# Optimization experiments

Hardware: AMD Instinct MI355X
Metric: run time of the kernel (lower is better)

The kernel has to match this reference:

```python
import jax, jax.numpy as jnp
import numpy as np

N = 8192      # num nodes
E = 131072    # num edges (avg degree 16)
B = 2         # batch
F_NODE = 128
F_EDGE = 64
H = 256       # hidden_dim
L = 3         # num_layers


def setup_inputs() -> dict:
    key = jax.random.key(0)
    ks = jax.random.split(key, 16)
    # unique edges, sorted row-major to match the original i-then-j loop order
    rng = np.random.default_rng(0)
    lin = np.sort(rng.choice(N * N, size=E, replace=False))
    src = jnp.asarray(lin // N, dtype=jnp.int32)
    dst = jnp.asarray(lin % N, dtype=jnp.int32)
    adjacency = jnp.zeros((N, N), jnp.float32).at[src, dst].set(1.0)

    s = 0.05
    return {
        "node_features": jax.random.normal(ks[0], (B, N, F_NODE), jnp.float32),
        "edge_features": jax.random.normal(ks[1], (B, E, F_EDGE), jnp.float32),
        "adjacency": adjacency,
        "src_idx": src,
        "dst_idx": dst,
        "W_ne": jax.random.normal(ks[2], (F_NODE, H), jnp.float32) * s,
        "b_ne": jnp.zeros((H,), jnp.float32),
        "W_ee": jax.random.normal(ks[3], (F_EDGE, H), jnp.float32) * s,
        "b_ee": jnp.zeros((H,), jnp.float32),
        "W_conv": jax.random.normal(ks[4], (L, H, H), jnp.float32) * s,
        "b_conv": jnp.zeros((L, H), jnp.float32),
        "W_cls": jax.random.normal(ks[5], (H, 5), jnp.float32) * s,
        "b_cls": jnp.zeros((5,), jnp.float32),
        "W_ep": jax.random.normal(ks[6], (2 * H, 1), jnp.float32) * s,
        "b_ep": jnp.zeros((1,), jnp.float32),
        "W_gp": jax.random.normal(ks[7], (H, 1), jnp.float32) * s,
        "b_gp": jnp.zeros((1,), jnp.float32),
    }


def reference(node_features, edge_features, adjacency, src_idx, dst_idx,
              W_ne, b_ne, W_ee, b_ee, W_conv, b_conv,
              W_cls, b_cls, W_ep, b_ep, W_gp, b_gp):
    # embeddings (eval mode: dropout is identity)
    h = jax.nn.relu(node_features @ W_ne + b_ne)          # [B,N,H]
    e = jax.nn.relu(edge_features @ W_ee + b_ee)          # [B,E,H] (computed, unused downstream as in original)
    # message-passing layers: messages = A @ h, then linear+relu+residual
    for l in range(L):
        m = jnp.einsum('ij,bjh->bih', adjacency, h)       # dense adjacency matmul
        o = jax.nn.relu(m @ W_conv[l] + b_conv[l])
        h = o + h                                          # residual (in==out dim)
    node_health = h @ W_cls + b_cls                        # [B,N,5]
    # fused edge prediction over all nonzero adjacency entries (row-major order)
    h_src = h[:, src_idx, :]                               # [B,E,H]
    h_dst = h[:, dst_idx, :]                               # [B,E,H]
    edge_repr = jnp.concatenate([h_src, h_dst], axis=-1)   # [B,E,2H]
    edge_propagation = jax.nn.sigmoid(edge_repr @ W_ep + b_ep)  # [B,E,1]
    global_repr = jnp.mean(h, axis=1)                      # [B,H]
    system_health = jax.nn.sigmoid(global_repr @ W_gp + b_gp)   # [B,1]
    return (node_health, edge_propagation, system_health, h)
```

## Files before the change

kernel.cpp:

```cpp
#include <hip/hip_runtime.h>
#include <hip/hip_bf16.h>

typedef __bf16 bf16_t;
typedef __bf16 bf16x8 __attribute__((ext_vector_type(8)));
typedef float f32x4 __attribute__((ext_vector_type(4)));

#define N_NODES 8192
#define N_EDGES 131072
#define HDIM    256


__device__ inline int rowblk_swz(int x) {
  int xcd = x & 7, q = x >> 3;
  return (xcd >> 2) * 128 + (xcd & 3) * 32 + q;
}

__device__ inline float wred(float v) {
#pragma unroll
  for (int m = 32; m; m >>= 1) v += __shfl_xor(v, m);
  return v;
}

__global__ __launch_bounds__(256) void gemm1_prep_k(const float* __restrict__ nf,
                                                    const float* __restrict__ Wne,
                                                    const float* __restrict__ bne,
                                                    const float* __restrict__ Wconv,
                                                    const int* __restrict__ src,
                                                    int* __restrict__ rp,
                                                    bf16_t* __restrict__ WconvT,
                                                    bf16_t* __restrict__ hs0) {
  __shared__ char smem[64 * 65 * 4];
  int x = blockIdx.x, tid = threadIdx.x;
  if (x >= 1024) {
    if (x < 1057) {
      int i = (x - 1024) * 256 + tid;
      if (i < N_NODES) {
        int lo = 0, hi = N_EDGES;
        while (lo < hi) { int mid = (lo + hi) >> 1; if (src[mid] < i) lo = mid + 1; else hi = mid; }
        rp[i] = lo;
      } else if (i == N_NODES) {
        rp[i] = N_EDGES;
      }
    } else {
      float (*tl)[65] = (float(*)[65])smem;
      int t = x - 1057;
      int l = t >> 4, tile = t & 15;
      int tr = (tile >> 2) * 64, tc = (tile & 3) * 64;
      int j = tid & 63, i0 = tid >> 6;
#pragma unroll
      for (int s = 0; s < 16; ++s) {
        int i = 4 * s + i0;
        tl[i][j] = Wconv[l * 65536 + (tr + i) * 256 + tc + j];
      }
      __syncthreads();
#pragma unroll
      for (int s = 0; s < 16; ++s) {
        int i = 4 * s + i0;
        WconvT[l * 65536 + (tc + i) * 256 + tr + j] = (bf16_t)tl[j][i];
      }
    }
    return;
  }
  bf16_t* Wlds = (bf16_t*)smem;
  int xb = x & 255, yb = x >> 8;
  int cg0 = yb * 64;
  for (int k = tid >> 6; k < 128; k += 4) {
    int lc = tid & 63;
    float w = Wne[k * 256 + cg0 + lc];
    Wlds[lc * 128 + (((k >> 3) ^ (lc & 15)) << 3) + (k & 7)] = (bf16_t)w;
  }
  int lane = tid & 63, wv = tid >> 6;
  int r0 = (rowblk_swz(xb) * 4 + wv) * 16;
  int l15 = lane & 15, l4 = lane >> 4;
  bf16x8 a[4];
  const float* Ap = nf + (size_t)(r0 + l15) * 128 + 8 * l4;
#pragma unroll
  for (int kk = 0; kk < 4; ++kk) {
    f32x4 a0 = *(const f32x4*)(Ap + 32 * kk);
    f32x4 a1 = *(const f32x4*)(Ap + 32 * kk + 4);
#pragma unroll
    for (int j = 0; j < 4; ++j) { a[kk][j] = (bf16_t)a0[j]; a[kk][4 + j] = (bf16_t)a1[j]; }
  }
  __syncthreads();
#pragma unroll
  for (int ct = 0; ct < 4; ++ct) {
    int lc0 = ct * 16;
    f32x4 acc = {0.f, 0.f, 0.f, 0.f};
#pragma unroll
    for (int kk = 0; kk < 4; ++kk) {
      bf16x8 b = *(const bf16x8*)&Wlds[(lc0 + l15) * 128 + (((4 * kk + l4) ^ l15) << 3)];
      acc = __builtin_amdgcn_mfma_f32_16x16x32_bf16(a[kk], b, acc, 0, 0, 0);
    }
    int col = cg0 + lc0 + l15;
    float bv = bne[col];
#pragma unroll
    for (int i = 0; i < 4; ++i) {
      int row = r0 + 4 * l4 + i;
      size_t idx = (size_t)row * HDIM + col;
      hs0[idx] = (bf16_t)fmaxf(acc[i] + bv, 0.f);
    }
  }
}

__global__ __launch_bounds__(512) void gconv_k(const bf16_t* __restrict__ hs_in,
                                               const int* __restrict__ rp,
                                               const int* __restrict__ dst,
                                               const bf16_t* __restrict__ BT,
                                               const float* __restrict__ bias,
                                               bf16_t* __restrict__ hs_out) {
  __shared__ bf16_t A_lds[32 * 256];
  int tid = threadIdx.x;
  int x = blockIdx.x;
  int xcd = x & 7, q = x >> 3;
  int b = xcd >> 2;
  int blk = (xcd & 3) * 64 + q;
  int i0 = blk * 32;
  int gang = tid >> 5, l32 = tid & 31;
  const bf16_t* hb = hs_in + (size_t)b * (N_NODES * HDIM) + l32 * 8;
#pragma unroll
  for (int r2 = 0; r2 < 2; ++r2) {
    int lrow = gang * 2 + r2;
    int i = i0 + lrow;
    int e0 = rp[i], e1 = rp[i + 1];
    float acc[8] = {0.f, 0.f, 0.f, 0.f, 0.f, 0.f, 0.f, 0.f};
    int e = e0;
    for (; e + 8 <= e1; e += 8) {
      bf16x8 v[8];
#pragma unroll
      for (int u = 0; u < 8; ++u) v[u] = *(const bf16x8*)(hb + (size_t)dst[e + u] * HDIM);
#pragma unroll
      for (int u = 0; u < 8; ++u)
#pragma unroll
        for (int jj = 0; jj < 8; ++jj) acc[jj] += (float)v[u][jj];
    }
    for (; e < e1; ++e) {
      bf16x8 v = *(const bf16x8*)(hb + (size_t)dst[e] * HDIM);
#pragma unroll
      for (int jj = 0; jj < 8; ++jj) acc[jj] += (float)v[jj];
    }
    bf16x8 o;
#pragma unroll
    for (int jj = 0; jj < 8; ++jj) o[jj] = (bf16_t)acc[jj];
    *(bf16x8*)&A_lds[lrow * 256 + ((l32 ^ (lrow & 7)) * 8)] = o;
  }
  __syncthreads();
  int lane = tid & 63, wv = tid >> 6;
  int wr = wv >> 2, wc = wv & 3;
  int l15 = lane & 15, l4 = lane >> 4;
  bf16x8 a[8];
#pragma unroll
  for (int kk = 0; kk < 8; ++kk)
    a[kk] = *(const bf16x8*)&A_lds[(wr * 16 + l15) * 256 + (((kk * 4 + l4) ^ (l15 & 7)) * 8)];
  int row_base = b * N_NODES + i0 + wr * 16;
#pragma unroll
  for (int ct = 0; ct < 4; ++ct) {
    int c0 = wc * 64 + ct * 16;
    const bf16_t* Bp = BT + (size_t)(c0 + l15) * HDIM + 8 * l4;
    f32x4 acc = {0.f, 0.f, 0.f, 0.f};
#pragma unroll
    for (int kk = 0; kk < 8; ++kk)
      acc = __builtin_amdgcn_mfma_f32_16x16x32_bf16(a[kk], *(const bf16x8*)(Bp + 32 * kk), acc, 0, 0, 0);
    int col = c0 + l15;
    float bv = bias[col];
#pragma unroll
    for (int ii = 0; ii < 4; ++ii) {
      int row = row_base + 4 * l4 + ii;
      size_t idx = (size_t)row * HDIM + col;
      float v = fmaxf(acc[ii] + bv, 0.f) + (float)hs_in[idx];
      hs_out[idx] = (bf16_t)v;
    }
  }
}

__global__ __launch_bounds__(512) void gconv_heads_k(const bf16_t* __restrict__ hs_in,
                                                     const int* __restrict__ rp,
                                                     const int* __restrict__ dst,
                                                     const bf16_t* __restrict__ BT,
                                                     const float* __restrict__ bias,
                                                     float* __restrict__ out_h,
                                                     const float* __restrict__ Wcls,
                                                     const float* __restrict__ bcls,
                                                     const float* __restrict__ Wep,
                                                     const float* __restrict__ Wgp,
                                                     float* __restrict__ ds,
                                                     float* __restrict__ dd,
                                                     float* __restrict__ pg,
                                                     float* __restrict__ out_nh) {
  __shared__ bf16_t A_lds[32 * 256];
  __shared__ float red[2][4][16][8];
  __shared__ float pgrow[32];
  int tid = threadIdx.x;
  int x = blockIdx.x;
  int xcd = x & 7, q = x >> 3;
  int b = xcd >> 2;
  int blk = (xcd & 3) * 64 + q;
  int i0 = blk * 32;
  int gang = tid >> 5, l32 = tid & 31;
  const bf16_t* hb = hs_in + (size_t)b * (N_NODES * HDIM) + l32 * 8;
#pragma unroll
  for (int r2 = 0; r2 < 2; ++r2) {
    int lrow = gang * 2 + r2;
    int i = i0 + lrow;
    int e0 = rp[i], e1 = rp[i + 1];
    float acc[8] = {0.f, 0.f, 0.f, 0.f, 0.f, 0.f, 0.f, 0.f};
    int e = e0;
    for (; e + 8 <= e1; e += 8) {
      bf16x8 v[8];
#pragma unroll
      for (int u = 0; u < 8; ++u) v[u] = *(const bf16x8*)(hb + (size_t)dst[e + u] * HDIM);
#pragma unroll
      for (int u = 0; u < 8; ++u)
#pragma unroll
        for (int jj = 0; jj < 8; ++jj) acc[jj] += (float)v[u][jj];
    }
    for (; e < e1; ++e) {
      bf16x8 v = *(const bf16x8*)(hb + (size_t)dst[e] * HDIM);
#pragma unroll
      for (int jj = 0; jj < 8; ++jj) acc[jj] += (float)v[jj];
    }
    bf16x8 o;
#pragma unroll
    for (int jj = 0; jj < 8; ++jj) o[jj] = (bf16_t)acc[jj];
    *(bf16x8*)&A_lds[lrow * 256 + ((l32 ^ (lrow & 7)) * 8)] = o;
  }
  __syncthreads();
  int lane = tid & 63, wv = tid >> 6;
  int wr = wv >> 2, wc = wv & 3;
  int l15 = lane & 15, l4 = lane >> 4;
  bf16x8 a[8];
#pragma unroll
  for (int kk = 0; kk < 8; ++kk)
    a[kk] = *(const bf16x8*)&A_lds[(wr * 16 + l15) * 256 + (((kk * 4 + l4) ^ (l15 & 7)) * 8)];
  int row_base = b * N_NODES + i0 + wr * 16;
  float p[4][8];
#pragma unroll
  for (int ii = 0; ii < 4; ++ii)
#pragma unroll
    for (int hh = 0; hh < 8; ++hh) p[ii][hh] = 0.f;
#pragma unroll
  for (int ct = 0; ct < 4; ++ct) {
    int c0 = wc * 64 + ct * 16;
    const bf16_t* Bp = BT + (size_t)(c0 + l15) * HDIM + 8 * l4;
    f32x4 acc = {0.f, 0.f, 0.f, 0.f};
#pragma unroll
    for (int kk = 0; kk < 8; ++kk)
      acc = __builtin_amdgcn_mfma_f32_16x16x32_bf16(a[kk], *(const bf16x8*)(Bp + 32 * kk), acc, 0, 0, 0);
    int col = c0 + l15;
    float bv = bias[col];
    float wc0 = Wcls[col * 5 + 0], wc1 = Wcls[col * 5 + 1], wc2 = Wcls[col * 5 + 2];
    float wc3 = Wcls[col * 5 + 3], wc4 = Wcls[col * 5 + 4];
    float wes = Wep[col], wed = Wep[256 + col], wgv = Wgp[col];
#pragma unroll
    for (int ii = 0; ii < 4; ++ii) {
      int row = row_base + 4 * l4 + ii;
      size_t idx = (size_t)row * HDIM + col;
      float v = fmaxf(acc[ii] + bv, 0.f) + (float)hs_in[idx];
      out_h[idx] = v;
      p[ii][0] += v * wc0; p[ii][1] += v * wc1; p[ii][2] += v * wc2;
      p[ii][3] += v * wc3; p[ii][4] += v * wc4;
      p[ii][5] += v * wes; p[ii][6] += v * wed; p[ii][7] += v * wgv;
    }
  }
#pragma unroll
  for (int ii = 0; ii < 4; ++ii)
#pragma unroll
    for (int hh = 0; hh < 8; ++hh) {
      float v = p[ii][hh];
#pragma unroll
      for (int m = 8; m; m >>= 1) v += __shfl_xor(v, m);
      p[ii][hh] = v;
    }
  if (l15 == 0) {
#pragma unroll
    for (int ii = 0; ii < 4; ++ii)
#pragma unroll
      for (int hh = 0; hh < 8; ++hh) red[wr][wc][4 * l4 + ii][hh] = p[ii][hh];
  }
  __syncthreads();
  if (tid < 256) {
    int rl = tid >> 3, hh = tid & 7;
    float s = red[rl >> 4][0][rl & 15][hh] + red[rl >> 4][1][rl & 15][hh] +
              red[rl >> 4][2][rl & 15][hh] + red[rl >> 4][3][rl & 15][hh];
    int grow = b * N_NODES + i0 + rl;
    if (hh < 5)      out_nh[(size_t)grow * 5 + hh] = s + bcls[hh];
    else if (hh == 5) ds[grow] = s;
    else if (hh == 6) dd[grow] = s;
    else              pgrow[rl] = s;
  }
  __syncthreads();
  if (tid == 0) {
    float t = 0.f;
#pragma unroll
    for (int rl = 0; rl < 32; ++rl) t += pgrow[rl];
    pg[b * 256 + blk] = t;
  }
}

__global__ __launch_bounds__(256) void edge_sys_k(const float* __restrict__ ds,
                                                  const float* __restrict__ dd,
                                                  const int* __restrict__ src,
                                                  const int* __restrict__ dst,
                                                  const float* __restrict__ bep,
                                                  const float* __restrict__ pg,
                                                  const float* __restrict__ bgp,
                                                  float* __restrict__ out_ep,
                                                  float* __restrict__ out_sys) {
  int x = blockIdx.x;
  if (x < 1024) {
    int t = x * 256 + threadIdx.x;
    int b = t >> 17;
    int e = t & (N_EDGES - 1);
    float v = ds[(b << 13) + src[e]] + dd[(b << 13) + dst[e]] + bep[0];
    out_ep[t] = 1.f / (1.f + expf(-v));
  } else {
    int b = x - 1024, t = threadIdx.x;
    float v = pg[b * 256 + t];
    v = wred(v);
    __shared__ float sm[4];
    if ((t & 63) == 0) sm[t >> 6] = v;
    __syncthreads();
    if (t == 0) {
      float tot = sm[0] + sm[1] + sm[2] + sm[3];
      float g = tot / (float)N_NODES + bgp[0];
      out_sys[b] = 1.f / (1.f + expf(-g));
    }
  }
}

extern "C" void kernel_launch(void* const* d_in, const int* in_sizes, int n_in,
                              void* d_out, int out_size, void* d_ws, size_t ws_size,
                              hipStream_t stream) {
  (void)in_sizes; (void)n_in; (void)out_size; (void)ws_size;
  const float* nf    = (const float*)d_in[0];
  const int*   src   = (const int*)d_in[3];
  const int*   dst   = (const int*)d_in[4];
  const float* Wne   = (const float*)d_in[5];
  const float* bne   = (const float*)d_in[6];
  const float* Wconv = (const float*)d_in[9];
  const float* bconv = (const float*)d_in[10];
  const float* Wcls  = (const float*)d_in[11];
  const float* bcls  = (const float*)d_in[12];
  const float* Wep   = (const float*)d_in[13];
  const float* bep   = (const float*)d_in[14];
  const float* Wgp   = (const float*)d_in[15];
  const float* bgp   = (const float*)d_in[16];

  char* ws = (char*)d_ws;
  bf16_t* hs0    = (bf16_t*)(ws + 0);
  bf16_t* hs1    = (bf16_t*)(ws + 8388608);
  bf16_t* WconvT = (bf16_t*)(ws + 16777216);
  int*    rp     = (int*)(ws + 17170432);
  float*  ds     = (float*)(ws + 17207296);
  float*  dd     = (float*)(ws + 17272832);
  float*  pg     = (float*)(ws + 17338368);

  float* out     = (float*)d_out;
  float* out_nh  = out;
  float* out_ep  = out + 81920;
  float* out_sys = out + 344064;
  float* out_h   = out + 344066;

  hipLaunchKernelGGL(gemm1_prep_k, dim3(1105), dim3(256), 0, stream,
                     nf, Wne, bne, Wconv, src, rp, WconvT, hs0);
  hipLaunchKernelGGL(gconv_k, dim3(512), dim3(512), 0, stream,
                     hs0, rp, dst, WconvT, bconv, hs1);
  hipLaunchKernelGGL(gconv_k, dim3(512), dim3(512), 0, stream,
                     hs1, rp, dst, WconvT + 65536, bconv + 256, hs0);
  hipLaunchKernelGGL(gconv_heads_k, dim3(512), dim3(512), 0, stream,
                     hs0, rp, dst, WconvT + 131072, bconv + 512, out_h,
                     Wcls, bcls, Wep, Wgp, ds, dd, pg, out_nh);
  hipLaunchKernelGGL(edge_sys_k, dim3(1026), dim3(256), 0, stream, ds, dd, src, dst, bep,
                     pg, bgp, out_ep, out_sys);
}
```

Measured before the change: 114.0 us.

## Use LDS work-queue to assign gather rows to whole wavefronts dynamically

Replaces the static assignment of two rows per 32-lane gang with a dynamic queue: each 64-lane wavefront atomically claims the next row from a shared counter and gathers it with 4-element bf16 loads per lane. This is meant to balance uneven row degrees across the eight waves in a block and shorten the wait at the barrier before the MFMA phase. In exchange it adds LDS atomics, a shuffle and an extra barrier per block, and uses narrower 8-byte loads instead of 16-byte loads.

```diff
diff --git a/kernel.cpp b/kernel.cpp
--- a/kernel.cpp
+++ b/kernel.cpp
@@ -2,6 +2,7 @@
 #include <hip/hip_bf16.h>
 
 typedef __bf16 bf16_t;
+typedef __bf16 bf16x4 __attribute__((ext_vector_type(4)));
 typedef __bf16 bf16x8 __attribute__((ext_vector_type(8)));
 typedef float f32x4 __attribute__((ext_vector_type(4)));
 
@@ -19,6 +20,41 @@
 #pragma unroll
   for (int m = 32; m; m >>= 1) v += __shfl_xor(v, m);
   return v;
+}
+
+__device__ inline void gather_phase(bf16_t* __restrict__ A_lds, int* qctr,
+                                    const bf16_t* __restrict__ hs_in,
+                                    const int* __restrict__ rp,
+                                    const int* __restrict__ dst,
+                                    int b, int i0, int tid) {
+  int l = tid & 63;
+  const bf16_t* hb = hs_in + (size_t)b * (N_NODES * HDIM) + l * 4;
+  for (;;) {
+    int lrow;
+    if (l == 0) lrow = atomicAdd(qctr, 1);
+    lrow = __shfl(lrow, 0);
+    if (lrow >= 32) break;
+    int i = i0 + lrow;
+    int e0 = rp[i], e1 = rp[i + 1];
+    float a0 = 0.f, a1 = 0.f, a2 = 0.f, a3 = 0.f;
+    int e = e0;
+    for (; e + 8 <= e1; e += 8) {
+      bf16x4 v[8];
+#pragma unroll
+      for (int u = 0; u < 8; ++u) v[u] = *(const bf16x4*)(hb + (size_t)dst[e + u] * HDIM);
+#pragma unroll
+      for (int u = 0; u < 8; ++u) {
+        a0 += (float)v[u][0]; a1 += (float)v[u][1];
+        a2 += (float)v[u][2]; a3 += (float)v[u][3];
+      }
+    }
+    for (; e < e1; ++e) {
+      bf16x4 v = *(const bf16x4*)(hb + (size_t)dst[e] * HDIM);
+      a0 += (float)v[0]; a1 += (float)v[1]; a2 += (float)v[2]; a3 += (float)v[3];
+    }
+    bf16x4 o; o[0] = (bf16_t)a0; o[1] = (bf16_t)a1; o[2] = (bf16_t)a2; o[3] = (bf16_t)a3;
+    *(bf16x4*)&A_lds[lrow * 256 + (((l >> 1) ^ (lrow & 7)) * 8) + (l & 1) * 4] = o;
+  }
 }
 
 __global__ __launch_bounds__(256) void gemm1_prep_k(const float* __restrict__ nf,
@@ -109,40 +145,16 @@
                                                const float* __restrict__ bias,
                                                bf16_t* __restrict__ hs_out) {
   __shared__ bf16_t A_lds[32 * 256];
+  __shared__ int qctr;
   int tid = threadIdx.x;
   int x = blockIdx.x;
   int xcd = x & 7, q = x >> 3;
   int b = xcd >> 2;
   int blk = (xcd & 3) * 64 + q;
   int i0 = blk * 32;
-  int gang = tid >> 5, l32 = tid & 31;
-  const bf16_t* hb = hs_in + (size_t)b * (N_NODES * HDIM) + l32 * 8;
-#pragma unroll
-  for (int r2 = 0; r2 < 2; ++r2) {
-    int lrow = gang * 2 + r2;
-    int i = i0 + lrow;
-    int e0 = rp[i], e1 = rp[i + 1];
-    float acc[8] = {0.f, 0.f, 0.f, 0.f, 0.f, 0.f, 0.f, 0.f};
-    int e = e0;
-    for (; e + 8 <= e1; e += 8) {
-      bf16x8 v[8];
-#pragma unroll
-      for (int u = 0; u < 8; ++u) v[u] = *(const bf16x8*)(hb + (size_t)dst[e + u] * HDIM);
-#pragma unroll
-      for (int u = 0; u < 8; ++u)
-#pragma unroll
-        for (int jj = 0; jj < 8; ++jj) acc[jj] += (float)v[u][jj];
-    }
-    for (; e < e1; ++e) {
-      bf16x8 v = *(const bf16x8*)(hb + (size_t)dst[e] * HDIM);
-#pragma unroll
-      for (int jj = 0; jj < 8; ++jj) acc[jj] += (float)v[jj];
-    }
-    bf16x8 o;
-#pragma unroll
-    for (int jj = 0; jj < 8; ++jj) o[jj] = (bf16_t)acc[jj];
-    *(bf16x8*)&A_lds[lrow * 256 + ((l32 ^ (lrow & 7)) * 8)] = o;
-  }
+  if (tid == 0) qctr = 0;
+  __syncthreads();
+  gather_phase(A_lds, &qctr, hs_in, rp, dst, b, i0, tid);
   __syncthreads();
   int lane = tid & 63, wv = tid >> 6;
   int wr = wv >> 2, wc = wv & 3;
@@ -187,6 +199,7 @@
                                                      float* __restrict__ pg,
                                                      float* __restrict__ out_nh) {
   __shared__ bf16_t A_lds[32 * 256];
+  __shared__ int qctr;
   __shared__ float red[2][4][16][8];
   __shared__ float pgrow[32];
   int tid = threadIdx.x;
@@ -195,34 +208,9 @@
   int b = xcd >> 2;
   int blk = (xcd & 3) * 64 + q;
   int i0 = blk * 32;
-  int gang = tid >> 5, l32 = tid & 31;
-  const bf16_t* hb = hs_in + (size_t)b * (N_NODES * HDIM) + l32 * 8;
-#pragma unroll
-  for (int r2 = 0; r2 < 2; ++r2) {
-    int lrow = gang * 2 + r2;
-    int i = i0 + lrow;
-    int e0 = rp[i], e1 = rp[i + 1];
-    float acc[8] = {0.f, 0.f, 0.f, 0.f, 0.f, 0.f, 0.f, 0.f};
-    int e = e0;
-    for (; e + 8 <= e1; e += 8) {
-      bf16x8 v[8];
-#pragma unroll
-      for (int u = 0; u < 8; ++u) v[u] = *(const bf16x8*)(hb + (size_t)dst[e + u] * HDIM);
-#pragma unroll
-      for (int u = 0; u < 8; ++u)
-#pragma unroll
-        for (int jj = 0; jj < 8; ++jj) acc[jj] += (float)v[u][jj];
-    }
-    for (; e < e1; ++e) {
-      bf16x8 v = *(const bf16x8*)(hb + (size_t)dst[e] * HDIM);
-#pragma unroll
-      for (int jj = 0; jj < 8; ++jj) acc[jj] += (float)v[jj];
-    }
-    bf16x8 o;
-#pragma unroll
-    for (int jj = 0; jj < 8; ++jj) o[jj] = (bf16_t)acc[jj];
-    *(bf16x8*)&A_lds[lrow * 256 + ((l32 ^ (lrow & 7)) * 8)] = o;
-  }
+  if (tid == 0) qctr = 0;
+  __syncthreads();
+  gather_phase(A_lds, &qctr, hs_in, rp, dst, b, i0, tid);
   __syncthreads();
   int lane = tid & 63, wv = tid >> 6;
   int wr = wv >> 2, wc = wv & 3;
```

After: 130.3 us. +14.2%, slower.
